# Optimization experiments

Hardware: AMD Instinct MI355X
Metric: run time of the kernel (lower is better)

The kernel has to match this reference:

```python
import jax, jax.numpy as jnp
import numpy as np

B, C, H, W = 16, 256, 64, 64
K = 1024

def setup_inputs() -> dict:
    key = jax.random.key(0)
    k1, k2 = jax.random.split(key)
    x = jax.random.normal(k1, (B, C, H, W), dtype=jnp.float32)
    codebook = jax.random.normal(k2, (K, C), dtype=jnp.float32)
    return {"x": x, "codebook": codebook}


def reference(x, codebook):
    b, c, h, w = x.shape
    # (B, C, H, W) -> (B*H*W, C)
    xf = jnp.transpose(x, (0, 2, 3, 1)).reshape(-1, c)
    # Squared euclidean distances to codebook (argmin is the same as for cdist).
    x2 = jnp.sum(xf * xf, axis=-1, keepdims=True)          # (N, 1)
    c2 = jnp.sum(codebook * codebook, axis=-1)               # (K,)
    dist = x2 - 2.0 * jnp.einsum('nc,kc->nk', xf, codebook) + c2  # (N, K)
    idx = jnp.argmin(dist, axis=-1)                          # (N,)
    quant = codebook[idx]                                     # (N, C)
    commitment_loss = jnp.mean((jax.lax.stop_gradient(quant) - xf) ** 2)
    codebook_loss = jnp.mean((quant - jax.lax.stop_gradient(xf)) ** 2)
    # Straight-through estimator
    quant_out = xf + jax.lax.stop_gradient(quant - xf)
    quant_out = jnp.transpose(quant_out.reshape(b, h, w, c), (0, 3, 1, 2))
    indices = idx.reshape(b, h, w)
    return quant_out, codebook_loss, commitment_loss, indices
```

## Files before the change

kernel.cpp:

```cpp
#include <hip/hip_runtime.h>

constexpr int Bn = 16, Cd = 256, Hn = 64, Wn = 64, Kc = 1024;
constexpr int QUANT_ELEMS = Bn * Hn * Wn * Cd;
constexpr int LOSS_OFF = QUANT_ELEMS;
constexpr int IDX_OFF = QUANT_ELEMS + 2;

typedef _Float16 half8 __attribute__((ext_vector_type(8)));
typedef float f32x4 __attribute__((ext_vector_type(4)));

constexpr size_t WS_CBFH = 0;
constexpr size_t WS_CBFL = 512 * 1024;
constexpr size_t WS_C2   = 1024 * 1024;
constexpr size_t WS_CBT  = 1024 * 1024 + 8192;

__global__ __launch_bounds__(256) void prep(const float* __restrict__ cb,
                                            float* __restrict__ cbT,
                                            _Float16* __restrict__ cbFh,
                                            _Float16* __restrict__ cbFl,
                                            float* __restrict__ c2,
                                            float* __restrict__ out) {
    __shared__ float cbs[16][257];
    const int tid = threadIdx.x;
    const int k0 = blockIdx.x * 16;
    {
        const int c4 = (tid & 63) * 4;
        const int r0 = tid >> 6;
        #pragma unroll
        for (int it = 0; it < 4; ++it) {
            const int r = r0 + it * 4;
            const float4 v = *(const float4*)&cb[(size_t)(k0 + r) * Cd + c4];
            cbs[r][c4] = v.x; cbs[r][c4 + 1] = v.y; cbs[r][c4 + 2] = v.z; cbs[r][c4 + 3] = v.w;
        }
    }
    __syncthreads();
    {
        const int kk = tid & 15, j0 = tid >> 4;
        for (int j = j0; j < 256; j += 16)
            cbT[(size_t)j * Kc + k0 + kk] = cbs[kk][j];
    }
    {
        const int i = tid >> 4, part = tid & 15;
        float s = 0.f;
        #pragma unroll
        for (int c = part * 16; c < part * 16 + 16; ++c) { const float v = cbs[i][c]; s += v * v; }
        s += __shfl_xor(s, 1);
        s += __shfl_xor(s, 2);
        s += __shfl_xor(s, 4);
        s += __shfl_xor(s, 8);
        if (part == 0) c2[k0 + i] = s;
    }
    for (int t = tid; t < 512; t += 256) {
        const int kblk = t >> 6;
        const int l = t & 63;
        const int code_l = l & 15;
        const int cbase = kblk * 32 + (l >> 4) * 8;
        half8 hv, lv;
        #pragma unroll
        for (int j = 0; j < 8; ++j) {
            const float v = cbs[code_l][cbase + j];
            const _Float16 hh = (_Float16)v;
            hv[j] = hh;
            lv[j] = (_Float16)(v - (float)hh);
        }
        const size_t e = (size_t)(blockIdx.x * 8 + kblk) * 64 + l;
        *(half8*)(cbFh + e * 8) = hv;
        *(half8*)(cbFl + e * 8) = lv;
    }
    if (blockIdx.x == 0 && tid == 0) {
        out[LOSS_OFF] = 0.f; out[LOSS_OFF + 1] = 0.f;
    }
}

__global__ __launch_bounds__(256, 3) void vq_main(const float* __restrict__ x,
                                                  const _Float16* __restrict__ cbFh,
                                                  const _Float16* __restrict__ cbFl,
                                                  const float* __restrict__ c2,
                                                  const float* __restrict__ cb,
                                                  const float* __restrict__ cbT,
                                                  float* __restrict__ out) {
    __shared__ half8 Axh[2048];
    __shared__ float q1ds[4][64];
    __shared__ int   q1is[4][64];
    __shared__ float q2ds[4][64];
    __shared__ int   idx_s[64];
    __shared__ float red[4];
    __shared__ int   flg[64];
    __shared__ int   nflag;

    float* xs  = (float*)Axh;
    float* dsm = xs + 256;
    int*   kkm = (int*)(dsm + 256);

    const int tid = threadIdx.x;
    const int lane = tid & 63;
    const int wv = tid >> 6;
    const int bh = blockIdx.x;
    const int b = bh >> 6, h = bh & 63;

    if (tid == 0) nflag = 0;

    {
        const int m = tid & 15;
        const int q = (tid >> 4) & 3;
        const int mt = tid >> 6;
        const int w = mt * 16 + m;
        const float* xb = x + ((size_t)b * Cd * Hn + h) * Wn + w;
        #pragma unroll
        for (int kblk = 0; kblk < 8; ++kblk) {
            half8 hv;
            #pragma unroll
            for (int j = 0; j < 8; ++j) {
                const int c = kblk * 32 + q * 8 + j;
                const float v = xb[(size_t)c * (Hn * Wn)];
                hv[j] = (_Float16)v;
            }
            Axh[(kblk * 4 + mt) * 64 + (q * 16 + m)] = hv;
        }
    }
    __syncthreads();

    float q1d[16], q2d[16];
    int   q1i[16];
    #pragma unroll
    for (int i = 0; i < 16; ++i) { q1d[i] = 3.4e38f; q2d[i] = 3.4e38f; q1i[i] = 0; }

    #pragma unroll 1
    for (int grp = 0; grp < 8; ++grp) {
        f32x4 acc[4][2];
        #pragma unroll
        for (int mt = 0; mt < 4; ++mt)
            #pragma unroll
            for (int nt = 0; nt < 2; ++nt) acc[mt][nt] = (f32x4){0.f, 0.f, 0.f, 0.f};

        #pragma unroll 2
        for (int kblk = 0; kblk < 8; ++kblk) {
            half8 bhf[2], blf[2];
            #pragma unroll
            for (int nt = 0; nt < 2; ++nt) {
                const int ntile = wv * 16 + grp * 2 + nt;
                const size_t be = ((size_t)(ntile * 8 + kblk) * 64 + lane) * 8;
                bhf[nt] = *(const half8*)(cbFh + be);
                blf[nt] = *(const half8*)(cbFl + be);
            }
            half8 ahf[4];
            #pragma unroll
            for (int mt = 0; mt < 4; ++mt)
                ahf[mt] = Axh[(kblk * 4 + mt) * 64 + lane];
            #pragma unroll
            for (int nt = 0; nt < 2; ++nt)
                #pragma unroll
                for (int mt = 0; mt < 4; ++mt)
                    acc[mt][nt] = __builtin_amdgcn_mfma_f32_16x16x32_f16(ahf[mt], bhf[nt], acc[mt][nt], 0, 0, 0);
            #pragma unroll
            for (int nt = 0; nt < 2; ++nt)
                #pragma unroll
                for (int mt = 0; mt < 4; ++mt)
                    acc[mt][nt] = __builtin_amdgcn_mfma_f32_16x16x32_f16(ahf[mt], blf[nt], acc[mt][nt], 0, 0, 0);
        }

        #pragma unroll
        for (int nt = 0; nt < 2; ++nt) {
            const int code = (wv * 16 + grp * 2 + nt) * 16 + (lane & 15);
            const float c2v = c2[code];
            #pragma unroll
            for (int mt = 0; mt < 4; ++mt) {
                #pragma unroll
                for (int reg = 0; reg < 4; ++reg) {
                    const float d = fmaf(-2.f, acc[mt][nt][reg], c2v);
                    const int qi = mt * 4 + reg;
                    const bool better = d < q1d[qi];
                    const float second = better ? q1d[qi] : d;
                    q2d[qi] = fminf(q2d[qi], second);
                    q1i[qi] = better ? code : q1i[qi];
                    q1d[qi] = fminf(q1d[qi], d);
                }
            }
        }
    }

    #pragma unroll
    for (int off = 1; off < 16; off <<= 1) {
        #pragma unroll
        for (int qi = 0; qi < 16; ++qi) {
            const float od1 = __shfl_xor(q1d[qi], off);
            const int   oi1 = __shfl_xor(q1i[qi], off);
            const float od2 = __shfl_xor(q2d[qi], off);
            const bool obetter = od1 < q1d[qi];
            const float loser = obetter ? q1d[qi] : od1;
            q2d[qi] = fminf(fminf(q2d[qi], od2), loser);
            q1d[qi] = obetter ? od1 : q1d[qi];
            q1i[qi] = obetter ? oi1 : q1i[qi];
        }
    }
    if ((lane & 15) == 0) {
        #pragma unroll
        for (int qi = 0; qi < 16; ++qi) {
            const int mt = qi >> 2, reg = qi & 3;
            const int row = mt * 16 + (lane >> 4) * 4 + reg;
            q1ds[wv][row] = q1d[qi];
            q1is[wv][row] = q1i[qi];
            q2ds[wv][row] = q2d[qi];
        }
    }
    __syncthreads();
    if (tid < 64) {
        float d1 = q1ds[0][tid]; int i1 = q1is[0][tid]; float d2 = q2ds[0][tid];
        #pragma unroll
        for (int v = 1; v < 4; ++v) {
            const float od1 = q1ds[v][tid]; const int oi1 = q1is[v][tid]; const float od2 = q2ds[v][tid];
            const bool obetter = od1 < d1;
            const float loser = obetter ? d1 : od1;
            d2 = fminf(fminf(d2, od2), loser);
            d1 = obetter ? od1 : d1;
            i1 = obetter ? oi1 : i1;
        }
        idx_s[tid] = i1;
        if (d2 - d1 < 0.12f) {
            const int pos = atomicAdd(&nflag, 1);
            flg[pos] = tid;
        }
    }
    __syncthreads();

    const int nf = nflag;
    for (int fi = 0; fi < nf; ++fi) {
        const int wrow = flg[fi];
        xs[tid] = x[(((size_t)b * Cd + tid) * Hn + h) * Wn + wrow];
        __syncthreads();
        float dot[4] = {0.f, 0.f, 0.f, 0.f};
        #pragma unroll 8
        for (int c = 0; c < Cd; ++c) {
            const float4 v = ((const float4*)(cbT + (size_t)c * Kc))[tid];
            const float xc = xs[c];
            dot[0] = fmaf(v.x, xc, dot[0]);
            dot[1] = fmaf(v.y, xc, dot[1]);
            dot[2] = fmaf(v.z, xc, dot[2]);
            dot[3] = fmaf(v.w, xc, dot[3]);
        }
        float bd = 3.4e38f; int bk = 0;
        #pragma unroll
        for (int j = 0; j < 4; ++j) {
            const int k = tid * 4 + j;
            const float d = c2[k] - 2.f * dot[j];
            if (d < bd) { bd = d; bk = k; }
        }
        dsm[tid] = bd; kkm[tid] = bk;
        __syncthreads();
        for (int s = 128; s > 0; s >>= 1) {
            if (tid < s) {
                const float od = dsm[tid + s]; const int ok = kkm[tid + s];
                if (od < dsm[tid] || (od == dsm[tid] && ok < kkm[tid])) { dsm[tid] = od; kkm[tid] = ok; }
            }
            __syncthreads();
        }
        if (tid == 0) idx_s[wrow] = kkm[0];
        __syncthreads();
    }

    if (tid < 64) out[IDX_OFF + bh * 64 + tid] = (float)idx_s[tid];

    {
        const int w = tid & 63;
        const int cq = wv;
        const int myidx = idx_s[w];
        const float4* cbrow = (const float4*)(cb + (size_t)myidx * Cd + cq * 64);
        const float* xrow = x + (((size_t)b * Cd + cq * 64) * Hn + h) * Wn + w;
        float* orow = out + (((size_t)b * Cd + cq * 64) * Hn + h) * Wn + w;
        float lsum = 0.f;
        #pragma unroll
        for (int i = 0; i < 16; ++i) {
            const float4 qv4 = cbrow[i];
            const size_t c0 = (size_t)(i * 4) * (Hn * Wn);
            const float xv0 = xrow[c0];
            const float xv1 = xrow[c0 + 1 * (Hn * Wn)];
            const float xv2 = xrow[c0 + 2 * (Hn * Wn)];
            const float xv3 = xrow[c0 + 3 * (Hn * Wn)];
            const float d0 = qv4.x - xv0, d1 = qv4.y - xv1, d2 = qv4.z - xv2, d3 = qv4.w - xv3;
            lsum += d0 * d0 + d1 * d1 + d2 * d2 + d3 * d3;
            orow[c0] = qv4.x;
            orow[c0 + 1 * (Hn * Wn)] = qv4.y;
            orow[c0 + 2 * (Hn * Wn)] = qv4.z;
            orow[c0 + 3 * (Hn * Wn)] = qv4.w;
        }
        #pragma unroll
        for (int off = 32; off >= 1; off >>= 1) lsum += __shfl_xor(lsum, off);
        if (lane == 0) red[wv] = lsum;
    }
    __syncthreads();
    if (tid == 0) {
        const float s = (red[0] + red[1] + red[2] + red[3]) * (1.0f / 16777216.0f);
        atomicAdd(out + LOSS_OFF, s);
        atomicAdd(out + LOSS_OFF + 1, s);
    }
}

extern "C" void kernel_launch(void* const* d_in, const int* in_sizes, int n_in,
                              void* d_out, int out_size, void* d_ws, size_t ws_size,
                              hipStream_t stream) {
    const float* x  = (const float*)d_in[0];
    const float* cb = (const float*)d_in[1];
    float* out = (float*)d_out;
    char* ws = (char*)d_ws;
    _Float16* cbFh = (_Float16*)(ws + WS_CBFH);
    _Float16* cbFl = (_Float16*)(ws + WS_CBFL);
    float* c2      = (float*)(ws + WS_C2);
    float* cbT     = (float*)(ws + WS_CBT);

    prep<<<64, 256, 0, stream>>>(cb, cbT, cbFh, cbFl, c2, out);
    vq_main<<<Bn * Hn, 256, 0, stream>>>(x, cbFh, cbFl, c2, cb, cbT, out);
}
```

Before: 256.0 us.

## Split x into fp16 hi/lo, drop fp32 fallback GEMV, track top-2 indices

Splits the input x into fp16 high and low parts and adds a third MFMA pass (x_lo times codebook_hi), which makes the distances accurate enough to shrink the ambiguity threshold from 0.12 to 1e-4. Ambiguous rows no longer run a full fp32 GEMV against the transposed codebook. Instead the kernel tracks the second-best index and re-checks only the top two candidates with an exact squared-error comparison on a single wave. It also prefetches the codebook fragments one step ahead, reads x back from LDS in the epilogue instead of from global memory, and removes the cbT transpose from prep. In exchange it does 50% more MFMA work, doubles the LDS used for A, and lowers the occupancy hint from 3 to 2 blocks per CU.

```diff
diff --git a/kernel.cpp b/kernel.cpp
--- a/kernel.cpp
+++ b/kernel.cpp
@@ -11,10 +11,10 @@
 constexpr size_t WS_CBFH = 0;
 constexpr size_t WS_CBFL = 512 * 1024;
 constexpr size_t WS_C2   = 1024 * 1024;
-constexpr size_t WS_CBT  = 1024 * 1024 + 8192;
+
+constexpr float THR = 1e-4f;
 
 __global__ __launch_bounds__(256) void prep(const float* __restrict__ cb,
-                                            float* __restrict__ cbT,
                                             _Float16* __restrict__ cbFh,
                                             _Float16* __restrict__ cbFl,
                                             float* __restrict__ c2,
@@ -34,11 +34,6 @@
     }
     __syncthreads();
     {
-        const int kk = tid & 15, j0 = tid >> 4;
-        for (int j = j0; j < 256; j += 16)
-            cbT[(size_t)j * Kc + k0 + kk] = cbs[kk][j];
-    }
-    {
         const int i = tid >> 4, part = tid & 15;
         float s = 0.f;
         #pragma unroll
@@ -71,25 +66,22 @@
     }
 }
 
-__global__ __launch_bounds__(256, 3) void vq_main(const float* __restrict__ x,
+__global__ __launch_bounds__(256, 2) void vq_main(const float* __restrict__ x,
                                                   const _Float16* __restrict__ cbFh,
                                                   const _Float16* __restrict__ cbFl,
                                                   const float* __restrict__ c2,
                                                   const float* __restrict__ cb,
-                                                  const float* __restrict__ cbT,
                                                   float* __restrict__ out) {
     __shared__ half8 Axh[2048];
+    __shared__ half8 Axl[2048];
     __shared__ float q1ds[4][64];
     __shared__ int   q1is[4][64];
     __shared__ float q2ds[4][64];
+    __shared__ int   q2is[4][64];
     __shared__ int   idx_s[64];
     __shared__ float red[4];
     __shared__ int   flg[64];
     __shared__ int   nflag;
-
-    float* xs  = (float*)Axh;
-    float* dsm = xs + 256;
-    int*   kkm = (int*)(dsm + 256);
 
     const int tid = threadIdx.x;
     const int lane = tid & 63;
@@ -107,55 +99,82 @@
         const float* xb = x + ((size_t)b * Cd * Hn + h) * Wn + w;
         #pragma unroll
         for (int kblk = 0; kblk < 8; ++kblk) {
-            half8 hv;
+            half8 hv, lv;
             #pragma unroll
             for (int j = 0; j < 8; ++j) {
                 const int c = kblk * 32 + q * 8 + j;
                 const float v = xb[(size_t)c * (Hn * Wn)];
-                hv[j] = (_Float16)v;
-            }
-            Axh[(kblk * 4 + mt) * 64 + (q * 16 + m)] = hv;
+                const _Float16 hh = (_Float16)v;
+                hv[j] = hh;
+                lv[j] = (_Float16)(v - (float)hh);
+            }
+            const int e = (kblk * 4 + mt) * 64 + (q * 16 + m);
+            Axh[e] = hv;
+            Axl[e] = lv;
         }
     }
     __syncthreads();
 
     float q1d[16], q2d[16];
-    int   q1i[16];
+    int   q1i[16], q2i[16];
     #pragma unroll
-    for (int i = 0; i < 16; ++i) { q1d[i] = 3.4e38f; q2d[i] = 3.4e38f; q1i[i] = 0; }
+    for (int i = 0; i < 16; ++i) { q1d[i] = 3.4e38f; q2d[i] = 3.4e38f; q1i[i] = 0; q2i[i] = 0; }
+
+    half8 nbh[2], nbl[2];
+    #pragma unroll
+    for (int nt = 0; nt < 2; ++nt) {
+        const int ntile = wv * 16 + nt;
+        const size_t be = ((size_t)(ntile * 8) * 64 + lane) * 8;
+        nbh[nt] = *(const half8*)(cbFh + be);
+        nbl[nt] = *(const half8*)(cbFl + be);
+    }
 
     #pragma unroll 1
     for (int grp = 0; grp < 8; ++grp) {
         f32x4 acc[4][2];
         #pragma unroll
-        for (int mt = 0; mt < 4; ++mt)
-            #pragma unroll
-            for (int nt = 0; nt < 2; ++nt) acc[mt][nt] = (f32x4){0.f, 0.f, 0.f, 0.f};
+        for (int mt = 0; mt < 4; ++mt) {
+            acc[mt][0] = (f32x4){0.f, 0.f, 0.f, 0.f};
+            acc[mt][1] = (f32x4){0.f, 0.f, 0.f, 0.f};
+        }
 
         #pragma unroll 2
         for (int kblk = 0; kblk < 8; ++kblk) {
-            half8 bhf[2], blf[2];
-            #pragma unroll
-            for (int nt = 0; nt < 2; ++nt) {
-                const int ntile = wv * 16 + grp * 2 + nt;
-                const size_t be = ((size_t)(ntile * 8 + kblk) * 64 + lane) * 8;
-                bhf[nt] = *(const half8*)(cbFh + be);
-                blf[nt] = *(const half8*)(cbFl + be);
-            }
-            half8 ahf[4];
-            #pragma unroll
-            for (int mt = 0; mt < 4; ++mt)
-                ahf[mt] = Axh[(kblk * 4 + mt) * 64 + lane];
-            #pragma unroll
-            for (int nt = 0; nt < 2; ++nt)
+            const half8 cbh0 = nbh[0], cbh1 = nbh[1];
+            const half8 cbl0 = nbl[0], cbl1 = nbl[1];
+            {
+                const int nk = (kblk + 1) & 7;
+                const int ng = (grp + ((kblk + 1) >> 3)) & 7;
                 #pragma unroll
-                for (int mt = 0; mt < 4; ++mt)
-                    acc[mt][nt] = __builtin_amdgcn_mfma_f32_16x16x32_f16(ahf[mt], bhf[nt], acc[mt][nt], 0, 0, 0);
-            #pragma unroll
-            for (int nt = 0; nt < 2; ++nt)
-                #pragma unroll
-                for (int mt = 0; mt < 4; ++mt)
-                    acc[mt][nt] = __builtin_amdgcn_mfma_f32_16x16x32_f16(ahf[mt], blf[nt], acc[mt][nt], 0, 0, 0);
+                for (int nt = 0; nt < 2; ++nt) {
+                    const int ntile = wv * 16 + ng * 2 + nt;
+                    const size_t be = ((size_t)(ntile * 8 + nk) * 64 + lane) * 8;
+                    nbh[nt] = *(const half8*)(cbFh + be);
+                    nbl[nt] = *(const half8*)(cbFl + be);
+                }
+            }
+            half8 ahf[4], alf[4];
+            #pragma unroll
+            for (int mt = 0; mt < 4; ++mt) {
+                const int e = (kblk * 4 + mt) * 64 + lane;
+                ahf[mt] = Axh[e];
+                alf[mt] = Axl[e];
+            }
+            #pragma unroll
+            for (int mt = 0; mt < 4; ++mt) {
+                acc[mt][0] = __builtin_amdgcn_mfma_f32_16x16x32_f16(ahf[mt], cbh0, acc[mt][0], 0, 0, 0);
+                acc[mt][1] = __builtin_amdgcn_mfma_f32_16x16x32_f16(ahf[mt], cbh1, acc[mt][1], 0, 0, 0);
+            }
+            #pragma unroll
+            for (int mt = 0; mt < 4; ++mt) {
+                acc[mt][0] = __builtin_amdgcn_mfma_f32_16x16x32_f16(ahf[mt], cbl0, acc[mt][0], 0, 0, 0);
+                acc[mt][1] = __builtin_amdgcn_mfma_f32_16x16x32_f16(ahf[mt], cbl1, acc[mt][1], 0, 0, 0);
+            }
+            #pragma unroll
+            for (int mt = 0; mt < 4; ++mt) {
+                acc[mt][0] = __builtin_amdgcn_mfma_f32_16x16x32_f16(alf[mt], cbh0, acc[mt][0], 0, 0, 0);
+                acc[mt][1] = __builtin_amdgcn_mfma_f32_16x16x32_f16(alf[mt], cbh1, acc[mt][1], 0, 0, 0);
+            }
         }
 
         #pragma unroll
@@ -168,11 +187,12 @@
                 for (int reg = 0; reg < 4; ++reg) {
                     const float d = fmaf(-2.f, acc[mt][nt][reg], c2v);
                     const int qi = mt * 4 + reg;
-                    const bool better = d < q1d[qi];
-                    const float second = better ? q1d[qi] : d;
-                    q2d[qi] = fminf(q2d[qi], second);
-                    q1i[qi] = better ? code : q1i[qi];
-                    q1d[qi] = fminf(q1d[qi], d);
+                    const bool b1 = d < q1d[qi];
+                    const bool b2 = d < q2d[qi];
+                    q2d[qi] = b1 ? q1d[qi] : (b2 ? d : q2d[qi]);
+                    q2i[qi] = b1 ? q1i[qi] : (b2 ? code : q2i[qi]);
+                    q1d[qi] = b1 ? d : q1d[qi];
+                    q1i[qi] = b1 ? code : q1i[qi];
                 }
             }
         }
@@ -185,11 +205,18 @@
             const float od1 = __shfl_xor(q1d[qi], off);
             const int   oi1 = __shfl_xor(q1i[qi], off);
             const float od2 = __shfl_xor(q2d[qi], off);
-            const bool obetter = od1 < q1d[qi];
-            const float loser = obetter ? q1d[qi] : od1;
-            q2d[qi] = fminf(fminf(q2d[qi], od2), loser);
-            q1d[qi] = obetter ? od1 : q1d[qi];
-            q1i[qi] = obetter ? oi1 : q1i[qi];
+            const int   oi2 = __shfl_xor(q2i[qi], off);
+            const bool ob = od1 < q1d[qi];
+            const float ld = ob ? q1d[qi] : od1;
+            const int   li = ob ? q1i[qi] : oi1;
+            const bool o2 = od2 < q2d[qi];
+            const float md = o2 ? od2 : q2d[qi];
+            const int   mi = o2 ? oi2 : q2i[qi];
+            const bool lb = ld < md;
+            q2d[qi] = lb ? ld : md;
+            q2i[qi] = lb ? li : mi;
+            q1d[qi] = ob ? od1 : q1d[qi];
+            q1i[qi] = ob ? oi1 : q1i[qi];
         }
     }
     if ((lane & 15) == 0) {
@@ -200,87 +227,96 @@
             q1ds[wv][row] = q1d[qi];
             q1is[wv][row] = q1i[qi];
             q2ds[wv][row] = q2d[qi];
+            q2is[wv][row] = q2i[qi];
         }
     }
     __syncthreads();
     if (tid < 64) {
-        float d1 = q1ds[0][tid]; int i1 = q1is[0][tid]; float d2 = q2ds[0][tid];
+        float d1 = q1ds[0][tid]; int i1 = q1is[0][tid];
+        float d2 = q2ds[0][tid]; int i2 = q2is[0][tid];
         #pragma unroll
         for (int v = 1; v < 4; ++v) {
-            const float od1 = q1ds[v][tid]; const int oi1 = q1is[v][tid]; const float od2 = q2ds[v][tid];
-            const bool obetter = od1 < d1;
-            const float loser = obetter ? d1 : od1;
-            d2 = fminf(fminf(d2, od2), loser);
-            d1 = obetter ? od1 : d1;
-            i1 = obetter ? oi1 : i1;
+            const float od1 = q1ds[v][tid]; const int oi1 = q1is[v][tid];
+            const float od2 = q2ds[v][tid]; const int oi2 = q2is[v][tid];
+            const bool ob = od1 < d1;
+            const float ld = ob ? d1 : od1;
+            const int   li = ob ? i1 : oi1;
+            const bool o2 = od2 < d2;
+            const float md = o2 ? od2 : d2;
+            const int   mi = o2 ? oi2 : i2;
+            const bool lb = ld < md;
+            d2 = lb ? ld : md;
+            i2 = lb ? li : mi;
+            d1 = ob ? od1 : d1;
+            i1 = ob ? oi1 : i1;
         }
         idx_s[tid] = i1;
-        if (d2 - d1 < 0.12f) {
+        if (d2 - d1 < THR) {
             const int pos = atomicAdd(&nflag, 1);
-            flg[pos] = tid;
+            flg[pos] = tid | (i2 << 6);
         }
     }
     __syncthreads();
 
     const int nf = nflag;
     for (int fi = 0; fi < nf; ++fi) {
-        const int wrow = flg[fi];
-        xs[tid] = x[(((size_t)b * Cd + tid) * Hn + h) * Wn + wrow];
-        __syncthreads();
-        float dot[4] = {0.f, 0.f, 0.f, 0.f};
-        #pragma unroll 8
-        for (int c = 0; c < Cd; ++c) {
-            const float4 v = ((const float4*)(cbT + (size_t)c * Kc))[tid];
-            const float xc = xs[c];
-            dot[0] = fmaf(v.x, xc, dot[0]);
-            dot[1] = fmaf(v.y, xc, dot[1]);
-            dot[2] = fmaf(v.z, xc, dot[2]);
-            dot[3] = fmaf(v.w, xc, dot[3]);
-        }
-        float bd = 3.4e38f; int bk = 0;
-        #pragma unroll
-        for (int j = 0; j < 4; ++j) {
-            const int k = tid * 4 + j;
-            const float d = c2[k] - 2.f * dot[j];
-            if (d < bd) { bd = d; bk = k; }
-        }
-        dsm[tid] = bd; kkm[tid] = bk;
-        __syncthreads();
-        for (int s = 128; s > 0; s >>= 1) {
-            if (tid < s) {
-                const float od = dsm[tid + s]; const int ok = kkm[tid + s];
-                if (od < dsm[tid] || (od == dsm[tid] && ok < kkm[tid])) { dsm[tid] = od; kkm[tid] = ok; }
-            }
-            __syncthreads();
-        }
-        if (tid == 0) idx_s[wrow] = kkm[0];
-        __syncthreads();
-    }
+        if (wv == 0) {
+            const int pack = flg[fi];
+            const int w = pack & 63;
+            const int i2 = pack >> 6;
+            const int i1 = idx_s[w];
+            const int mt = w >> 4, m = w & 15;
+            float s1 = 0.f, s2 = 0.f;
+            #pragma unroll
+            for (int cc = 0; cc < 4; ++cc) {
+                const int c = lane * 4 + cc;
+                const int kblk = c >> 5, q = (c >> 3) & 3, j = c & 7;
+                const int e = (kblk * 4 + mt) * 64 + q * 16 + m;
+                const float xv = (float)Axh[e][j] + (float)Axl[e][j];
+                const float e1 = cb[(size_t)i1 * Cd + c] - xv;
+                const float e2 = cb[(size_t)i2 * Cd + c] - xv;
+                s1 = fmaf(e1, e1, s1);
+                s2 = fmaf(e2, e2, s2);
+            }
+            #pragma unroll
+            for (int off = 32; off >= 1; off >>= 1) {
+                s1 += __shfl_xor(s1, off);
+                s2 += __shfl_xor(s2, off);
+            }
+            if (lane == 0 && (s2 < s1 || (s2 == s1 && i2 < i1))) idx_s[w] = i2;
+        }
+    }
+    __syncthreads();
 
     if (tid < 64) out[IDX_OFF + bh * 64 + tid] = (float)idx_s[tid];
 
     {
         const int w = tid & 63;
         const int cq = wv;
+        const int m = w & 15, mt = w >> 4;
         const int myidx = idx_s[w];
         const float4* cbrow = (const float4*)(cb + (size_t)myidx * Cd + cq * 64);
-        const float* xrow = x + (((size_t)b * Cd + cq * 64) * Hn + h) * Wn + w;
-        float* orow = out + (((size_t)b * Cd + cq * 64) * Hn + h) * Wn + w;
         float lsum = 0.f;
         #pragma unroll
-        for (int i = 0; i < 16; ++i) {
-            const float4 qv4 = cbrow[i];
-            const size_t c0 = (size_t)(i * 4) * (Hn * Wn);
-            const float xv0 = xrow[c0];
-            const float xv1 = xrow[c0 + 1 * (Hn * Wn)];
-            const float xv2 = xrow[c0 + 2 * (Hn * Wn)];
-            const float xv3 = xrow[c0 + 3 * (Hn * Wn)];
-            const float d0 = qv4.x - xv0, d1 = qv4.y - xv1, d2 = qv4.z - xv2, d3 = qv4.w - xv3;
-            lsum += d0 * d0 + d1 * d1 + d2 * d2 + d3 * d3;
-            orow[c0] = qv4.x;
-            orow[c0 + 1 * (Hn * Wn)] = qv4.y;
-            orow[c0 + 2 * (Hn * Wn)] = qv4.z;
-            orow[c0 + 3 * (Hn * Wn)] = qv4.w;
+        for (int half = 0; half < 2; ++half) {
+            const int kblk = cq * 2 + half;
+            #pragma unroll
+            for (int q = 0; q < 4; ++q) {
+                const int e = (kblk * 4 + mt) * 64 + q * 16 + m;
+                const half8 hv = Axh[e];
+                const half8 lv = Axl[e];
+                const float4 qa = cbrow[half * 8 + q * 2];
+                const float4 qb = cbrow[half * 8 + q * 2 + 1];
+                const float qv[8] = {qa.x, qa.y, qa.z, qa.w, qb.x, qb.y, qb.z, qb.w};
+                const int cbase = cq * 64 + half * 32 + q * 8;
+                #pragma unroll
+                for (int j = 0; j < 8; ++j) {
+                    const float xv = (float)hv[j] + (float)lv[j];
+                    const float dd = qv[j] - xv;
+                    lsum += dd * dd;
+                    out[(((size_t)b * Cd + cbase + j) * Hn + h) * Wn + w] = qv[j];
+                }
+            }
         }
         #pragma unroll
         for (int off = 32; off >= 1; off >>= 1) lsum += __shfl_xor(lsum, off);
@@ -304,8 +340,7 @@
     _Float16* cbFh = (_Float16*)(ws + WS_CBFH);
     _Float16* cbFl = (_Float16*)(ws + WS_CBFL);
     float* c2      = (float*)(ws + WS_C2);
-    float* cbT     = (float*)(ws + WS_CBT);
-
-    prep<<<64, 256, 0, stream>>>(cb, cbT, cbFh, cbFl, c2, out);
-    vq_main<<<Bn * Hn, 256, 0, stream>>>(x, cbFh, cbFl, c2, cb, cbT, out);
+
+    prep<<<64, 256, 0, stream>>>(cb, cbFh, cbFl, c2, out);
+    vq_main<<<Bn * Hn, 256, 0, stream>>>(x, cbFh, cbFl, c2, cb, out);
 }
```

Result: faster. 242.1 us (-5.4%).
